# Kernel tuning notes

Measured on AMD Instinct MI355X. Metric: run time of the kernel, lower is better.

The kernel has to match this reference:

```python
import jax, jax.numpy as jnp
import numpy as np

TOPK = 7  # hard-coded k in cal_high_score_instance_mask
EPS_DICE = 1e-8


def setup_inputs() -> dict:
    key = jax.random.key(0)
    k1, k2, k3, k4 = jax.random.split(key, 4)
    b, n, v, h, w = 4, 16, 32, 160, 160
    pred_mask = jax.random.normal(k1, (b, 1, h, w), dtype=jnp.float32)
    encode_feat = jax.random.normal(k2, (b, v, h, w), dtype=jnp.float32)
    gt_instances = (jax.random.uniform(k3, (b, n, h, w)) > 0.8).astype(jnp.float32)
    # validity mask over instance slots
    gt_index_mask = jax.random.randint(k4, (b, n), 0, 2).astype(jnp.int32)
    return {
        "pred_mask": pred_mask,
        "encode_feat": encode_feat,
        "gt_instances": gt_instances,
        "gt_index_mask": gt_index_mask,
    }


def reference(pred_mask, encode_feat, gt_instances, gt_index_mask):
    b, v, h, w = encode_feat.shape
    n = gt_instances.shape[1]
    hw = h * w
    feat = encode_feat.reshape(b, v, hw)          # b, v, hw
    gt = gt_instances.reshape(b, n, hw)           # b, n, hw
    valid = gt_index_mask.astype(feat.dtype)      # b, n  (0/1)

    # ---- get_mean_embedding_vector: masked mean of embedding per instance
    pix = jnp.clip(gt.sum(-1), 1.0)               # b, n
    mean_emb = jnp.einsum('bvp,bnp->bnv', feat, gt) / pix[..., None]

    # ---- cal_high_score_instance_mask: topk over masked score map, gather embeddings
    pre_regions = pred_mask.reshape(b, 1, hw) * gt             # b, n, hw
    _wvals, idx = jax.lax.top_k(pre_regions, TOPK)              # b, n, k
    idx_flat = idx.reshape(b, n * TOPK)                         # b, n*k
    # gather embedding vectors at topk pixel locations -> b, n*k, v
    idx_feat_th = jnp.take_along_axis(feat, idx_flat[:, None, :], axis=2)
    idx_feat_th = jnp.transpose(idx_feat_th, (0, 2, 1))

    # ---- get_isntance_mask: embedding-vector x feature-map matmuls
    inst_masks = jnp.einsum('bkv,bvp->bkp', idx_feat_th, feat)  # b, n*k, hw
    mean_masks = jnp.einsum('bnv,bvp->bnp', mean_emb, feat)     # b, n, hw

    # ---- w_dice_loss on mean-embedding masks (valid instances only)
    p_mean = jax.nn.sigmoid(mean_masks)
    denom_mean = jnp.clip((p_mean ** 2).sum(-1) + (gt ** 2).sum(-1), EPS_DICE)
    dice_mean = 1.0 - 2.0 * (gt * p_mean).sum(-1) / denom_mean  # b, n
    mean_inst_loss = (dice_mean * valid).sum()

    # ---- w_dice_loss on topk-instance masks (target expanded over k)
    p_k = jax.nn.sigmoid(inst_masks.reshape(b, n, TOPK, hw))
    t_k = gt[:, :, None, :]                                     # b, n, 1, hw
    denom_k = jnp.clip((p_k ** 2).sum(-1) + (t_k ** 2).sum(-1), EPS_DICE)
    dice_k = 1.0 - 2.0 * (t_k * p_k).sum(-1) / denom_k          # b, n, k
    inst_loss = (dice_k * valid[..., None]).sum()

    # ---- l2_loss: masked squared distance of per-pixel embedding to instance mean
    diff = (feat[:, None, :, :] - mean_emb[..., None]) * gt[:, :, None, :]  # b, n, v, hw
    l2 = (diff ** 2).sum(-1) / pix[..., None]                   # b, n, v
    embedding_l2_loss = (l2.sum(-1) * valid).sum()

    return jnp.stack([mean_inst_loss, inst_loss, embedding_l2_loss])
```

## Files before the change

kernel.cpp:

```cpp
#include <hip/hip_runtime.h>
#include <cstdint>
#include <cstddef>

#define B 4
#define N 16
#define V 32
#define HW 25600
#define TOPK 7
#define NSLB 5
#define NCA 200
#define NCC 400

__device__ __forceinline__ bool better(float av, int ai, float bv, int bi) {
    return (av > bv) || (av == bv && ai < bi);
}

__global__ __launch_bounds__(256) void kTop(
    const float* __restrict__ pred, const float* __restrict__ gt,
    float* __restrict__ cand_val, int* __restrict__ cand_idx,
    float* __restrict__ cnt_part) {
    int s = blockIdx.x;
    int bn = s / NSLB, sl = s % NSLB;
    int b = bn >> 4;
    int tid = threadIdx.x;
    int lane = tid & 63, wave = tid >> 6;
    int base = sl * 5120;

    const float* gtrow = gt + (size_t)bn * HW + base;
    const float* pr = pred + (size_t)b * HW + base;

    float tv[TOPK]; int ti[TOPK];
#pragma unroll
    for (int j = 0; j < TOPK; ++j) { tv[j] = -INFINITY; ti[j] = 0x7fffffff; }
    float cnt = 0.f;

#pragma unroll
    for (int it = 0; it < 5; ++it) {
        int p = it * 1024 + tid * 4;
        float4 g4 = *reinterpret_cast<const float4*>(gtrow + p);
        float4 p4 = *reinterpret_cast<const float4*>(pr + p);
        cnt += g4.x + g4.y + g4.z + g4.w;
        float ca[4] = { p4.x * g4.x, p4.y * g4.y, p4.z * g4.z, p4.w * g4.w };
#pragma unroll
        for (int j = 0; j < 4; ++j) {
            float c = ca[j]; int pi = base + p + j;
            if (better(c, pi, tv[TOPK - 1], ti[TOPK - 1])) {
                tv[TOPK - 1] = c; ti[TOPK - 1] = pi;
#pragma unroll
                for (int q = TOPK - 2; q >= 0; --q) {
                    if (better(tv[q + 1], ti[q + 1], tv[q], ti[q])) {
                        float fv = tv[q]; int fi = ti[q];
                        tv[q] = tv[q + 1]; ti[q] = ti[q + 1];
                        tv[q + 1] = fv; ti[q + 1] = fi;
                    }
                }
            }
        }
    }

    __shared__ float rwv[4];
    __shared__ int rwi[4];
    __shared__ float csum[4];

#pragma unroll
    for (int off = 32; off > 0; off >>= 1) cnt += __shfl_down(cnt, off);
    if (lane == 0) csum[wave] = cnt;
    __syncthreads();
    if (tid == 0) cnt_part[s] = csum[0] + csum[1] + csum[2] + csum[3];

    int cbase = s * TOPK;
    for (int r = 0; r < TOPK; ++r) {
        float bv = tv[0]; int bi = ti[0];
#pragma unroll
        for (int m = 1; m <= 32; m <<= 1) {
            float ov = __shfl_xor(bv, m);
            int oi = __shfl_xor(bi, m);
            if (better(ov, oi, bv, bi)) { bv = ov; bi = oi; }
        }
        if (lane == 0) { rwv[wave] = bv; rwi[wave] = bi; }
        __syncthreads();
        float fv = rwv[0]; int fi = rwi[0];
#pragma unroll
        for (int w = 1; w < 4; ++w)
            if (better(rwv[w], rwi[w], fv, fi)) { fv = rwv[w]; fi = rwi[w]; }
        if (ti[0] == fi) {
#pragma unroll
            for (int q = 0; q < TOPK - 1; ++q) { tv[q] = tv[q + 1]; ti[q] = ti[q + 1]; }
            tv[TOPK - 1] = -INFINITY; ti[TOPK - 1] = 0x7fffffff;
        }
        if (tid == 0) { cand_val[cbase + r] = fv; cand_idx[cbase + r] = fi; }
        __syncthreads();
    }
}

__global__ __launch_bounds__(256) void kA(
    const float* __restrict__ feat, const float* __restrict__ gt,
    float* __restrict__ ms_part, float* __restrict__ s2_part) {
    int s = blockIdx.x;
    int xcd = s & 7;
    int b = xcd >> 1;
    int ch = (s >> 3) * 2 + (xcd & 1);
    int c0 = ch * 128;
    int tid = threadIdx.x;
    int ng = tid >> 6, vg = (tid >> 3) & 7, pg = tid & 7;

    const float* gb = gt + (size_t)(b * N + ng * 4) * HW + c0 + pg * 4;
    const float* fb = feat + (size_t)(b * V + vg * 4) * HW + c0 + pg * 4;

    float acc[4][4];
#pragma unroll
    for (int i = 0; i < 4; ++i)
#pragma unroll
        for (int j = 0; j < 4; ++j) acc[i][j] = 0.f;
    float s2a[4] = { 0.f, 0.f, 0.f, 0.f };

#pragma unroll
    for (int q = 0; q < 4; ++q) {
        int p = q * 32;
        float4 g4[4], f4[4];
#pragma unroll
        for (int i = 0; i < 4; ++i)
            g4[i] = *reinterpret_cast<const float4*>(gb + (size_t)i * HW + p);
#pragma unroll
        for (int j = 0; j < 4; ++j)
            f4[j] = *reinterpret_cast<const float4*>(fb + (size_t)j * HW + p);
        float ffx = 0.f, ffy = 0.f, ffz = 0.f, ffw = 0.f;
#pragma unroll
        for (int j = 0; j < 4; ++j) {
            ffx = fmaf(f4[j].x, f4[j].x, ffx);
            ffy = fmaf(f4[j].y, f4[j].y, ffy);
            ffz = fmaf(f4[j].z, f4[j].z, ffz);
            ffw = fmaf(f4[j].w, f4[j].w, ffw);
        }
#pragma unroll
        for (int i = 0; i < 4; ++i) {
#pragma unroll
            for (int j = 0; j < 4; ++j) {
                acc[i][j] = fmaf(g4[i].x, f4[j].x, acc[i][j]);
                acc[i][j] = fmaf(g4[i].y, f4[j].y, acc[i][j]);
                acc[i][j] = fmaf(g4[i].z, f4[j].z, acc[i][j]);
                acc[i][j] = fmaf(g4[i].w, f4[j].w, acc[i][j]);
            }
            s2a[i] = fmaf(g4[i].x, ffx, s2a[i]);
            s2a[i] = fmaf(g4[i].y, ffy, s2a[i]);
            s2a[i] = fmaf(g4[i].z, ffz, s2a[i]);
            s2a[i] = fmaf(g4[i].w, ffw, s2a[i]);
        }
    }
#pragma unroll
    for (int m = 1; m <= 4; m <<= 1)
#pragma unroll
        for (int i = 0; i < 4; ++i)
#pragma unroll
            for (int j = 0; j < 4; ++j) acc[i][j] += __shfl_xor(acc[i][j], m);
    size_t blk = (size_t)(b * NCA + ch);
    if (pg == 0) {
        float* dst = ms_part + blk * 512;
#pragma unroll
        for (int i = 0; i < 4; ++i)
#pragma unroll
            for (int j = 0; j < 4; ++j)
                dst[(ng * 4 + i) * 32 + vg * 4 + j] = acc[i][j];
    }
#pragma unroll
    for (int m = 1; m <= 32; m <<= 1)
#pragma unroll
        for (int i = 0; i < 4; ++i) s2a[i] += __shfl_xor(s2a[i], m);
    if ((tid & 63) == 0) {
#pragma unroll
        for (int i = 0; i < 4; ++i)
            s2_part[blk * 16 + ng * 4 + i] = s2a[i];
    }
}

__global__ __launch_bounds__(256) void kB(
    const float* __restrict__ feat, const float* __restrict__ ms_part,
    const float* __restrict__ s2_part,
    const float* __restrict__ cand_val, const int* __restrict__ cand_idx,
    const float* __restrict__ cnt_part, const int* __restrict__ valid,
    float* __restrict__ Ebuf, float* __restrict__ cntbuf, float* __restrict__ out) {
    int bn = blockIdx.x;
    int b = bn >> 4, n = bn & 15;
    int tid = threadIdx.x;
    int lane = tid & 63, wave = tid >> 6;

    __shared__ int idx7[TOPK];
    __shared__ float msred[2][32];
    __shared__ float s2sh;

    if (wave == 0) {
        float cv = -INFINITY; int ci = 0x7fffffff;
        if (lane < NSLB * TOPK) {
            cv = cand_val[(size_t)bn * NSLB * TOPK + lane];
            ci = cand_idx[(size_t)bn * NSLB * TOPK + lane];
        }
#pragma unroll
        for (int r = 0; r < TOPK; ++r) {
            float bv = cv; int bi = ci;
#pragma unroll
            for (int m = 1; m <= 32; m <<= 1) {
                float ov = __shfl_xor(bv, m);
                int oi = __shfl_xor(bi, m);
                if (better(ov, oi, bv, bi)) { bv = ov; bi = oi; }
            }
            if (ci == bi) { cv = -INFINITY; ci = 0x7fffffff; }
            if (lane == 0) idx7[r] = bi;
        }
    } else if (wave <= 2) {
        int half = wave - 1;
        int v = lane & 31, hh = lane >> 5;
        int cstart = half * 100 + hh * 50;
        const float* src = ms_part + (size_t)b * NCA * 512 + n * 32 + v;
        float sm = 0.f;
        for (int k = 0; k < 50; ++k) sm += src[(size_t)(cstart + k) * 512];
        sm += __shfl_xor(sm, 32);
        if (lane < 32) msred[half][v] = sm;
    } else {
        float sv = 0.f;
        const float* src = s2_part + (size_t)b * NCA * 16 + n;
        for (int k = lane; k < NCA; k += 64) sv += src[(size_t)k * 16];
#pragma unroll
        for (int m = 1; m <= 32; m <<= 1) sv += __shfl_xor(sv, m);
        if (lane == 0) s2sh = sv;
    }
    __syncthreads();

    if (tid < 32) {
        const float* cp = cnt_part + bn * NSLB;
        float cnt = cp[0] + cp[1] + cp[2] + cp[3] + cp[4];
        float msum = msred[0][tid] + msred[1][tid];
        float pix = fmaxf(cnt, 1.0f);
        float mu = msum / pix;
        Ebuf[(size_t)bn * 256 + tid] = mu;
        float msq = mu * mu;
#pragma unroll
        for (int m = 1; m <= 16; m <<= 1) msq += __shfl_xor(msq, m);
        if (tid == 0) {
            cntbuf[bn] = cnt;
            float l2 = (s2sh / pix - msq) * (float)valid[bn];
            atomicAdd(out + 2, l2);
        }
    } else {
        int t = tid - 32;
        if (t < 224) {
            int r = t >> 5, v = t & 31;
            Ebuf[(size_t)bn * 256 + (r + 1) * 32 + v] =
                feat[((size_t)b * V + v) * HW + idx7[r]];
        }
    }
}

__global__ __launch_bounds__(256) void kC(
    const float* __restrict__ feat, const float* __restrict__ gt,
    const float* __restrict__ Ebuf, float* __restrict__ sums_part) {
    int s = blockIdx.x;
    int xcd = s & 7;
    int b = xcd >> 1;
    int ch = (s >> 3) * 2 + (xcd & 1);
    int c0 = ch * 64;
    int tid = threadIdx.x;
    int n = tid >> 4, pg = tid & 15;

    __shared__ float e_lds[8 * 16 * 36];
    __shared__ float red[16][17];

    const float* eb = Ebuf + (size_t)b * 4096;
#pragma unroll
    for (int k = 0; k < 16; ++k) {
        int q = tid + 256 * k;
        int nn = q >> 8, rr = (q >> 5) & 7, vv = q & 31;
        e_lds[(rr * 16 + nn) * 36 + vv] = eb[q];
    }
    __syncthreads();

    const float* fb = feat + (size_t)b * V * HW + c0 + pg * 4;
    float4 g4 = *reinterpret_cast<const float4*>(gt + (size_t)(b * N + n) * HW + c0 + pg * 4);

    float acc[8][4];
#pragma unroll
    for (int r = 0; r < 8; ++r)
#pragma unroll
        for (int j = 0; j < 4; ++j) acc[r][j] = 0.f;

    float4 c0_ = *reinterpret_cast<const float4*>(fb);
    float4 c1_ = *reinterpret_cast<const float4*>(fb + HW);
    float4 c2_ = *reinterpret_cast<const float4*>(fb + 2 * (size_t)HW);
    float4 c3_ = *reinterpret_cast<const float4*>(fb + 3 * (size_t)HW);
#pragma unroll
    for (int vq = 0; vq < 8; ++vq) {
        float4 n0_, n1_, n2_, n3_;
        if (vq < 7) {
            const float* np = fb + (size_t)(vq * 4 + 4) * HW;
            n0_ = *reinterpret_cast<const float4*>(np);
            n1_ = *reinterpret_cast<const float4*>(np + HW);
            n2_ = *reinterpret_cast<const float4*>(np + 2 * (size_t)HW);
            n3_ = *reinterpret_cast<const float4*>(np + 3 * (size_t)HW);
        }
#pragma unroll
        for (int r = 0; r < 8; ++r) {
            float4 e4 = *reinterpret_cast<const float4*>(&e_lds[(r * 16 + n) * 36 + vq * 4]);
            acc[r][0] = fmaf(e4.x, c0_.x, acc[r][0]);
            acc[r][0] = fmaf(e4.y, c1_.x, acc[r][0]);
            acc[r][0] = fmaf(e4.z, c2_.x, acc[r][0]);
            acc[r][0] = fmaf(e4.w, c3_.x, acc[r][0]);
            acc[r][1] = fmaf(e4.x, c0_.y, acc[r][1]);
            acc[r][1] = fmaf(e4.y, c1_.y, acc[r][1]);
            acc[r][1] = fmaf(e4.z, c2_.y, acc[r][1]);
            acc[r][1] = fmaf(e4.w, c3_.y, acc[r][1]);
            acc[r][2] = fmaf(e4.x, c0_.z, acc[r][2]);
            acc[r][2] = fmaf(e4.y, c1_.z, acc[r][2]);
            acc[r][2] = fmaf(e4.z, c2_.z, acc[r][2]);
            acc[r][2] = fmaf(e4.w, c3_.z, acc[r][2]);
            acc[r][3] = fmaf(e4.x, c0_.w, acc[r][3]);
            acc[r][3] = fmaf(e4.y, c1_.w, acc[r][3]);
            acc[r][3] = fmaf(e4.z, c2_.w, acc[r][3]);
            acc[r][3] = fmaf(e4.w, c3_.w, acc[r][3]);
        }
        if (vq < 7) { c0_ = n0_; c1_ = n1_; c2_ = n2_; c3_ = n3_; }
    }

    float p2[8], tp[8];
#pragma unroll
    for (int r = 0; r < 8; ++r) { p2[r] = 0.f; tp[r] = 0.f; }
    float ga[4] = { g4.x, g4.y, g4.z, g4.w };
#pragma unroll
    for (int r = 0; r < 8; ++r)
#pragma unroll
        for (int j = 0; j < 4; ++j) {
            float sg = 1.f / (1.f + __expf(-acc[r][j]));
            p2[r] = fmaf(sg, sg, p2[r]);
            tp[r] = fmaf(ga[j], sg, tp[r]);
        }
#pragma unroll
    for (int m = 1; m <= 8; m <<= 1)
#pragma unroll
        for (int r = 0; r < 8; ++r) {
            p2[r] += __shfl_xor(p2[r], m);
            tp[r] += __shfl_xor(tp[r], m);
        }
    if (pg == 0) {
#pragma unroll
        for (int r = 0; r < 8; ++r) {
            red[n][r * 2] = p2[r];
            red[n][r * 2 + 1] = tp[r];
        }
    }
    __syncthreads();
    sums_part[(size_t)(b * NCC + ch) * 256 + tid] = red[tid >> 4][tid & 15];
}

__global__ __launch_bounds__(256) void kD(
    const float* __restrict__ sums_part, const float* __restrict__ cntbuf,
    const int* __restrict__ valid, float* __restrict__ out) {
    int bn = blockIdx.x;
    int b = bn >> 4, n = bn & 15;
    int tid = threadIdx.x;
    int slot = tid & 15, cg = tid >> 4;
    int lane = tid & 63, wave = tid >> 6;

    __shared__ float red2[4][17];
    __shared__ float fin[16];

    float sv = 0.f;
    const float* src = sums_part + (size_t)b * NCC * 256 + n * 16 + slot;
    for (int k = 0; k < 25; ++k) sv += src[(size_t)(cg + 16 * k) * 256];
    sv += __shfl_xor(sv, 16);
    sv += __shfl_xor(sv, 32);
    if (lane < 16) red2[wave][lane] = sv;
    __syncthreads();
    if (tid < 16) fin[tid] = red2[0][tid] + red2[1][tid] + red2[2][tid] + red2[3][tid];
    __syncthreads();

    if (tid == 0) {
        float vw = (float)valid[bn];
        float cnt = cntbuf[bn];
        float mloss = 0.f, iloss = 0.f;
#pragma unroll
        for (int r = 0; r < 8; ++r) {
            float p2 = fin[r * 2];
            float tp = fin[r * 2 + 1];
            float denom = fmaxf(p2 + cnt, 1e-8f);
            float dice = 1.f - 2.f * tp / denom;
            if (r == 0) mloss = dice * vw;
            else iloss += dice * vw;
        }
        atomicAdd(out + 0, mloss);
        atomicAdd(out + 1, iloss);
    }
}

extern "C" void kernel_launch(void* const* d_in, const int* in_sizes, int n_in,
                              void* d_out, int out_size, void* d_ws, size_t ws_size,
                              hipStream_t stream) {
    const float* pred = (const float*)d_in[0];
    const float* feat = (const float*)d_in[1];
    const float* gtin = (const float*)d_in[2];
    const int* valid  = (const int*)d_in[3];
    float* out = (float*)d_out;

    char* ws = (char*)d_ws;
    float* ms_part   = (float*)(ws);
    float* s2_part   = (float*)(ws + 1638400);
    float* cand_val  = (float*)(ws + 1689600);
    int*   cand_idx  = (int*)  (ws + 1698560);
    float* cnt_part  = (float*)(ws + 1707520);
    float* sums_part = (float*)(ws + 1708800);
    float* Ebuf      = (float*)(ws + 3347200);
    float* cntbuf    = (float*)(ws + 3412736);

    hipMemsetAsync(out, 0, 3 * sizeof(float), stream);

    kTop<<<B * N * NSLB, 256, 0, stream>>>(pred, gtin, cand_val, cand_idx, cnt_part);
    kA<<<B * NCA, 256, 0, stream>>>(feat, gtin, ms_part, s2_part);
    kB<<<B * N, 256, 0, stream>>>(feat, ms_part, s2_part, cand_val, cand_idx,
                                  cnt_part, valid, Ebuf, cntbuf, out);
    kC<<<B * NCC, 256, 0, stream>>>(feat, gtin, Ebuf, sums_part);
    kD<<<B * N, 256, 0, stream>>>(sums_part, cntbuf, valid, out);
}
```

Baseline: 67.11 us.

## Fuse top-k candidate search into masked-mean pass and rework kB reduction

Removes the separate kTop kernel and computes per-chunk top-7 candidates and pixel counts inside the kA pass, which already reads the gt chunk, with pred staged in shared memory. kB now merges 200 chunk candidate lists per instance with a block-wide top-k and uses all 256 threads for the partial-sum reductions. kC's Ebuf staging into shared memory switches to float4 loads. This saves one launch and one full read of gt, but makes the candidate buffers much larger and adds a heavier serial merge to kB.

New measurement: 70.70 us. 5.3% more time.

```diff
diff --git a/kernel.cpp b/kernel.cpp
--- a/kernel.cpp
+++ b/kernel.cpp
@@ -7,7 +7,6 @@
 #define V 32
 #define HW 25600
 #define TOPK 7
-#define NSLB 5
 #define NCA 200
 #define NCC 400
 
@@ -15,95 +14,23 @@
     return (av > bv) || (av == bv && ai < bi);
 }
 
-__global__ __launch_bounds__(256) void kTop(
-    const float* __restrict__ pred, const float* __restrict__ gt,
-    float* __restrict__ cand_val, int* __restrict__ cand_idx,
-    float* __restrict__ cnt_part) {
-    int s = blockIdx.x;
-    int bn = s / NSLB, sl = s % NSLB;
-    int b = bn >> 4;
-    int tid = threadIdx.x;
-    int lane = tid & 63, wave = tid >> 6;
-    int base = sl * 5120;
-
-    const float* gtrow = gt + (size_t)bn * HW + base;
-    const float* pr = pred + (size_t)b * HW + base;
-
-    float tv[TOPK]; int ti[TOPK];
-#pragma unroll
-    for (int j = 0; j < TOPK; ++j) { tv[j] = -INFINITY; ti[j] = 0x7fffffff; }
-    float cnt = 0.f;
-
-#pragma unroll
-    for (int it = 0; it < 5; ++it) {
-        int p = it * 1024 + tid * 4;
-        float4 g4 = *reinterpret_cast<const float4*>(gtrow + p);
-        float4 p4 = *reinterpret_cast<const float4*>(pr + p);
-        cnt += g4.x + g4.y + g4.z + g4.w;
-        float ca[4] = { p4.x * g4.x, p4.y * g4.y, p4.z * g4.z, p4.w * g4.w };
-#pragma unroll
-        for (int j = 0; j < 4; ++j) {
-            float c = ca[j]; int pi = base + p + j;
-            if (better(c, pi, tv[TOPK - 1], ti[TOPK - 1])) {
-                tv[TOPK - 1] = c; ti[TOPK - 1] = pi;
-#pragma unroll
-                for (int q = TOPK - 2; q >= 0; --q) {
-                    if (better(tv[q + 1], ti[q + 1], tv[q], ti[q])) {
-                        float fv = tv[q]; int fi = ti[q];
-                        tv[q] = tv[q + 1]; ti[q] = ti[q + 1];
-                        tv[q + 1] = fv; ti[q + 1] = fi;
-                    }
-                }
-            }
-        }
-    }
-
-    __shared__ float rwv[4];
-    __shared__ int rwi[4];
-    __shared__ float csum[4];
-
-#pragma unroll
-    for (int off = 32; off > 0; off >>= 1) cnt += __shfl_down(cnt, off);
-    if (lane == 0) csum[wave] = cnt;
-    __syncthreads();
-    if (tid == 0) cnt_part[s] = csum[0] + csum[1] + csum[2] + csum[3];
-
-    int cbase = s * TOPK;
-    for (int r = 0; r < TOPK; ++r) {
-        float bv = tv[0]; int bi = ti[0];
-#pragma unroll
-        for (int m = 1; m <= 32; m <<= 1) {
-            float ov = __shfl_xor(bv, m);
-            int oi = __shfl_xor(bi, m);
-            if (better(ov, oi, bv, bi)) { bv = ov; bi = oi; }
-        }
-        if (lane == 0) { rwv[wave] = bv; rwi[wave] = bi; }
-        __syncthreads();
-        float fv = rwv[0]; int fi = rwi[0];
-#pragma unroll
-        for (int w = 1; w < 4; ++w)
-            if (better(rwv[w], rwi[w], fv, fi)) { fv = rwv[w]; fi = rwi[w]; }
-        if (ti[0] == fi) {
-#pragma unroll
-            for (int q = 0; q < TOPK - 1; ++q) { tv[q] = tv[q + 1]; ti[q] = ti[q + 1]; }
-            tv[TOPK - 1] = -INFINITY; ti[TOPK - 1] = 0x7fffffff;
-        }
-        if (tid == 0) { cand_val[cbase + r] = fv; cand_idx[cbase + r] = fi; }
-        __syncthreads();
-    }
-}
-
-__global__ __launch_bounds__(256) void kA(
-    const float* __restrict__ feat, const float* __restrict__ gt,
-    float* __restrict__ ms_part, float* __restrict__ s2_part) {
+__global__ __launch_bounds__(256) void kP1(
+    const float* __restrict__ pred, const float* __restrict__ feat,
+    const float* __restrict__ gt,
+    float* __restrict__ ms_part, float* __restrict__ s2_part,
+    float* __restrict__ cnt_part,
+    float* __restrict__ cand_val, int* __restrict__ cand_idx) {
     int s = blockIdx.x;
     int xcd = s & 7;
     int b = xcd >> 1;
     int ch = (s >> 3) * 2 + (xcd & 1);
     int c0 = ch * 128;
     int tid = threadIdx.x;
+
+    __shared__ float p_lds[128];
+    if (tid < 128) p_lds[tid] = pred[(size_t)b * HW + c0 + tid];
+
     int ng = tid >> 6, vg = (tid >> 3) & 7, pg = tid & 7;
-
     const float* gb = gt + (size_t)(b * N + ng * 4) * HW + c0 + pg * 4;
     const float* fb = feat + (size_t)(b * V + vg * 4) * HW + c0 + pg * 4;
 
@@ -171,64 +98,150 @@
         for (int i = 0; i < 4; ++i)
             s2_part[blk * 16 + ng * 4 + i] = s2a[i];
     }
+    __syncthreads();
+
+    {
+        int n = tid >> 4, si = tid & 15;
+        const float* gr = gt + (size_t)(b * N + n) * HW + c0;
+        float tv[TOPK]; int ti[TOPK];
+#pragma unroll
+        for (int j = 0; j < TOPK; ++j) { tv[j] = -INFINITY; ti[j] = 0x7fffffff; }
+        float cnt = 0.f;
+#pragma unroll
+        for (int k = 0; k < 8; ++k) {
+            int px = si + 16 * k;
+            float g = gr[px];
+            float c = p_lds[px] * g;
+            cnt += g;
+            int pi = c0 + px;
+            if (better(c, pi, tv[TOPK - 1], ti[TOPK - 1])) {
+                tv[TOPK - 1] = c; ti[TOPK - 1] = pi;
+#pragma unroll
+                for (int q = TOPK - 2; q >= 0; --q) {
+                    if (better(tv[q + 1], ti[q + 1], tv[q], ti[q])) {
+                        float fv = tv[q]; int fi = ti[q];
+                        tv[q] = tv[q + 1]; ti[q] = ti[q + 1];
+                        tv[q + 1] = fv; ti[q + 1] = fi;
+                    }
+                }
+            }
+        }
+#pragma unroll
+        for (int m = 1; m <= 8; m <<= 1) cnt += __shfl_xor(cnt, m);
+        if (si == 0) cnt_part[blk * 16 + n] = cnt;
+
+        size_t cb = blk * 112 + n * 7;
+#pragma unroll
+        for (int r = 0; r < TOPK; ++r) {
+            float bv = tv[0]; int bi = ti[0];
+#pragma unroll
+            for (int m = 1; m <= 8; m <<= 1) {
+                float ov = __shfl_xor(bv, m);
+                int oi = __shfl_xor(bi, m);
+                if (better(ov, oi, bv, bi)) { bv = ov; bi = oi; }
+            }
+            if (ti[0] == bi) {
+#pragma unroll
+                for (int q = 0; q < TOPK - 1; ++q) { tv[q] = tv[q + 1]; ti[q] = ti[q + 1]; }
+                tv[TOPK - 1] = -INFINITY; ti[TOPK - 1] = 0x7fffffff;
+            }
+            if (si == 0) { cand_val[cb + r] = bv; cand_idx[cb + r] = bi; }
+        }
+    }
 }
 
 __global__ __launch_bounds__(256) void kB(
     const float* __restrict__ feat, const float* __restrict__ ms_part,
-    const float* __restrict__ s2_part,
+    const float* __restrict__ s2_part, const float* __restrict__ cnt_part,
     const float* __restrict__ cand_val, const int* __restrict__ cand_idx,
-    const float* __restrict__ cnt_part, const int* __restrict__ valid,
+    const int* __restrict__ valid,
     float* __restrict__ Ebuf, float* __restrict__ cntbuf, float* __restrict__ out) {
     int bn = blockIdx.x;
     int b = bn >> 4, n = bn & 15;
     int tid = threadIdx.x;
     int lane = tid & 63, wave = tid >> 6;
 
+    __shared__ float msl[8][33];
+    __shared__ float s2w[4], cw[4];
+    __shared__ float rwv[4];
+    __shared__ int rwi[4];
     __shared__ int idx7[TOPK];
-    __shared__ float msred[2][32];
-    __shared__ float s2sh;
-
-    if (wave == 0) {
-        float cv = -INFINITY; int ci = 0x7fffffff;
-        if (lane < NSLB * TOPK) {
-            cv = cand_val[(size_t)bn * NSLB * TOPK + lane];
-            ci = cand_idx[(size_t)bn * NSLB * TOPK + lane];
-        }
-#pragma unroll
-        for (int r = 0; r < TOPK; ++r) {
-            float bv = cv; int bi = ci;
-#pragma unroll
-            for (int m = 1; m <= 32; m <<= 1) {
-                float ov = __shfl_xor(bv, m);
-                int oi = __shfl_xor(bi, m);
-                if (better(ov, oi, bv, bi)) { bv = ov; bi = oi; }
+
+    {
+        int sl = tid >> 5, v = tid & 31;
+        const float* src = ms_part + ((size_t)(b * NCA) + sl) * 512 + n * 32 + v;
+        float sm = 0.f;
+#pragma unroll 5
+        for (int k = 0; k < 25; ++k) sm += src[(size_t)(8 * k) * 512];
+        msl[sl][v] = sm;
+    }
+    {
+        float s2v = 0.f, cv_ = 0.f;
+        if (tid < NCA) {
+            s2v = s2_part[((size_t)(b * NCA) + tid) * 16 + n];
+            cv_ = cnt_part[((size_t)(b * NCA) + tid) * 16 + n];
+        }
+#pragma unroll
+        for (int m = 1; m <= 32; m <<= 1) {
+            s2v += __shfl_xor(s2v, m);
+            cv_ += __shfl_xor(cv_, m);
+        }
+        if (lane == 0) { s2w[wave] = s2v; cw[wave] = cv_; }
+    }
+    float tv[TOPK]; int ti[TOPK];
+#pragma unroll
+    for (int j = 0; j < TOPK; ++j) { tv[j] = -INFINITY; ti[j] = 0x7fffffff; }
+    {
+        const float* cvp = cand_val + (size_t)(b * NCA) * 112 + n * 7;
+        const int* cip = cand_idx + (size_t)(b * NCA) * 112 + n * 7;
+#pragma unroll
+        for (int k = 0; k < 6; ++k) {
+            int j = tid + 256 * k;
+            if (j < NCA * TOPK) {
+                int chq = j / 7, rq = j % 7;
+                float c = cvp[(size_t)chq * 112 + rq];
+                int ix = cip[(size_t)chq * 112 + rq];
+                if (better(c, ix, tv[TOPK - 1], ti[TOPK - 1])) {
+                    tv[TOPK - 1] = c; ti[TOPK - 1] = ix;
+#pragma unroll
+                    for (int q = TOPK - 2; q >= 0; --q) {
+                        if (better(tv[q + 1], ti[q + 1], tv[q], ti[q])) {
+                            float fv = tv[q]; int fi = ti[q];
+                            tv[q] = tv[q + 1]; ti[q] = ti[q + 1];
+                            tv[q + 1] = fv; ti[q + 1] = fi;
+                        }
+                    }
+                }
             }
-            if (ci == bi) { cv = -INFINITY; ci = 0x7fffffff; }
-            if (lane == 0) idx7[r] = bi;
-        }
-    } else if (wave <= 2) {
-        int half = wave - 1;
-        int v = lane & 31, hh = lane >> 5;
-        int cstart = half * 100 + hh * 50;
-        const float* src = ms_part + (size_t)b * NCA * 512 + n * 32 + v;
-        float sm = 0.f;
-        for (int k = 0; k < 50; ++k) sm += src[(size_t)(cstart + k) * 512];
-        sm += __shfl_xor(sm, 32);
-        if (lane < 32) msred[half][v] = sm;
-    } else {
-        float sv = 0.f;
-        const float* src = s2_part + (size_t)b * NCA * 16 + n;
-        for (int k = lane; k < NCA; k += 64) sv += src[(size_t)k * 16];
-#pragma unroll
-        for (int m = 1; m <= 32; m <<= 1) sv += __shfl_xor(sv, m);
-        if (lane == 0) s2sh = sv;
-    }
-    __syncthreads();
-
+        }
+    }
+    __syncthreads();
+    for (int r = 0; r < TOPK; ++r) {
+        float bv = tv[0]; int bi = ti[0];
+#pragma unroll
+        for (int m = 1; m <= 32; m <<= 1) {
+            float ov = __shfl_xor(bv, m);
+            int oi = __shfl_xor(bi, m);
+            if (better(ov, oi, bv, bi)) { bv = ov; bi = oi; }
+        }
+        if (lane == 0) { rwv[wave] = bv; rwi[wave] = bi; }
+        __syncthreads();
+        float fv = rwv[0]; int fi = rwi[0];
+#pragma unroll
+        for (int w = 1; w < 4; ++w)
+            if (better(rwv[w], rwi[w], fv, fi)) { fv = rwv[w]; fi = rwi[w]; }
+        if (ti[0] == fi) {
+#pragma unroll
+            for (int q = 0; q < TOPK - 1; ++q) { tv[q] = tv[q + 1]; ti[q] = ti[q + 1]; }
+            tv[TOPK - 1] = -INFINITY; ti[TOPK - 1] = 0x7fffffff;
+        }
+        if (tid == 0) idx7[r] = fi;
+        __syncthreads();
+    }
     if (tid < 32) {
-        const float* cp = cnt_part + bn * NSLB;
-        float cnt = cp[0] + cp[1] + cp[2] + cp[3] + cp[4];
-        float msum = msred[0][tid] + msred[1][tid];
+        float cnt = cw[0] + cw[1] + cw[2] + cw[3];
+        float msum = msl[0][tid] + msl[1][tid] + msl[2][tid] + msl[3][tid]
+                   + msl[4][tid] + msl[5][tid] + msl[6][tid] + msl[7][tid];
         float pix = fmaxf(cnt, 1.0f);
         float mu = msum / pix;
         Ebuf[(size_t)bn * 256 + tid] = mu;
@@ -237,8 +250,8 @@
         for (int m = 1; m <= 16; m <<= 1) msq += __shfl_xor(msq, m);
         if (tid == 0) {
             cntbuf[bn] = cnt;
-            float l2 = (s2sh / pix - msq) * (float)valid[bn];
-            atomicAdd(out + 2, l2);
+            float s2 = s2w[0] + s2w[1] + s2w[2] + s2w[3];
+            atomicAdd(out + 2, (s2 / pix - msq) * (float)valid[bn]);
         }
     } else {
         int t = tid - 32;
@@ -266,10 +279,11 @@
 
     const float* eb = Ebuf + (size_t)b * 4096;
 #pragma unroll
-    for (int k = 0; k < 16; ++k) {
-        int q = tid + 256 * k;
+    for (int k = 0; k < 4; ++k) {
+        int q = (tid + 256 * k) * 4;
         int nn = q >> 8, rr = (q >> 5) & 7, vv = q & 31;
-        e_lds[(rr * 16 + nn) * 36 + vv] = eb[q];
+        *reinterpret_cast<float4*>(&e_lds[(rr * 16 + nn) * 36 + vv]) =
+            *reinterpret_cast<const float4*>(eb + q);
     }
     __syncthreads();
 
@@ -401,19 +415,19 @@
     char* ws = (char*)d_ws;
     float* ms_part   = (float*)(ws);
     float* s2_part   = (float*)(ws + 1638400);
-    float* cand_val  = (float*)(ws + 1689600);
-    int*   cand_idx  = (int*)  (ws + 1698560);
-    float* cnt_part  = (float*)(ws + 1707520);
-    float* sums_part = (float*)(ws + 1708800);
-    float* Ebuf      = (float*)(ws + 3347200);
-    float* cntbuf    = (float*)(ws + 3412736);
+    float* cnt_part  = (float*)(ws + 1689600);
+    float* cand_val  = (float*)(ws + 1740800);
+    int*   cand_idx  = (int*)  (ws + 2099200);
+    float* sums_part = (float*)(ws + 2457600);
+    float* Ebuf      = (float*)(ws + 4096000);
+    float* cntbuf    = (float*)(ws + 4161536);
 
     hipMemsetAsync(out, 0, 3 * sizeof(float), stream);
 
-    kTop<<<B * N * NSLB, 256, 0, stream>>>(pred, gtin, cand_val, cand_idx, cnt_part);
-    kA<<<B * NCA, 256, 0, stream>>>(feat, gtin, ms_part, s2_part);
-    kB<<<B * N, 256, 0, stream>>>(feat, ms_part, s2_part, cand_val, cand_idx,
-                                  cnt_part, valid, Ebuf, cntbuf, out);
+    kP1<<<B * NCA, 256, 0, stream>>>(pred, feat, gtin, ms_part, s2_part,
+                                     cnt_part, cand_val, cand_idx);
+    kB<<<B * N, 256, 0, stream>>>(feat, ms_part, s2_part, cnt_part,
+                                  cand_val, cand_idx, valid, Ebuf, cntbuf, out);
     kC<<<B * NCC, 256, 0, stream>>>(feat, gtin, Ebuf, sums_part);
     kD<<<B * N, 256, 0, stream>>>(sums_part, cntbuf, valid, out);
 }
```
